# Kernel tuning notes

Measured on AMD Instinct MI355X. Metric: run time of the kernel, lower is better.

The kernel has to match this reference:

```python
import jax, jax.numpy as jnp
import numpy as np

C = 64
CQ = C // 8


def setup_inputs() -> dict:
    key = jax.random.key(0)
    ks = jax.random.split(key, 8)
    x = jax.random.normal(ks[0], (8, C, 64, 64), dtype=jnp.float32)
    s = 1.0 / np.sqrt(C)
    Wq = jax.random.normal(ks[1], (CQ, C), dtype=jnp.float32) * s
    bq = jax.random.normal(ks[2], (CQ,), dtype=jnp.float32) * s
    Wk = jax.random.normal(ks[3], (CQ, C), dtype=jnp.float32) * s
    bk = jax.random.normal(ks[4], (CQ,), dtype=jnp.float32) * s
    Wv = jax.random.normal(ks[5], (C, C), dtype=jnp.float32) * s
    bv = jax.random.normal(ks[6], (C,), dtype=jnp.float32) * s
    gamma = jnp.array([0.5], dtype=jnp.float32)  # nonzero so value path contributes
    return {"x": x, "Wq": Wq, "bq": bq, "Wk": Wk, "bk": bk, "Wv": Wv, "bv": bv, "gamma": gamma}


def reference(x, Wq, bq, Wk, bk, Wv, bv, gamma):
    B, Cc, H, W = x.shape
    xf = x.reshape(B, Cc, H * W)  # [B, C, N]
    # 1x1 conv == channel-mixing linear
    f = jnp.einsum('oc,bcn->bon', Wq, xf) + bq[None, :, None]  # [B, C/8, N]
    g = jnp.einsum('oc,bcn->bon', Wk, xf) + bk[None, :, None]  # [B, C/8, N]
    h = jnp.einsum('oc,bcn->bon', Wv, xf) + bv[None, :, None]  # [B, C, N]
    # scores[b,i,j] = f[b,:,i] . g[b,:,j]; softmax over dim=1 (query dim i)
    scores = jnp.einsum('bdi,bdj->bij', f, g)  # [B, N, N]
    beta = jax.nn.softmax(scores, axis=1)
    o = gamma[0] * jnp.einsum('bcn,bnm->bcm', h, beta) + xf
    return o.reshape(B, Cc, H, W)
```

## Files before the change

### kernel.cpp

```cpp
#include <hip/hip_runtime.h>
#include <hip/hip_fp16.h>


typedef _Float16 half8_t __attribute__((ext_vector_type(8)));
typedef _Float16 half4_t __attribute__((ext_vector_type(4)));
typedef _Float16 half2_t __attribute__((ext_vector_type(2)));
typedef __fp16  fp16x2  __attribute__((ext_vector_type(2)));
typedef float float4_t __attribute__((ext_vector_type(4)));
typedef unsigned int uintx4 __attribute__((ext_vector_type(4)));

#define NTOK 4096
#define PRH 72
#define LOG2E 1.44269504088896340736f

#if __has_builtin(__builtin_amdgcn_exp2f)
__device__ __forceinline__ float fexp2(float x) { return __builtin_amdgcn_exp2f(x); }
#else
__device__ __forceinline__ float fexp2(float x) { return exp2f(x); }
#endif

__device__ __forceinline__ half2_t pkcvt(float a, float b) {
    fp16x2 v = __builtin_amdgcn_cvt_pkrtz(a, b);
    return __builtin_bit_cast(half2_t, v);
}

__device__ __forceinline__ float4_t mfma16(half4_t a, half4_t b, float4_t c) {
    return __builtin_amdgcn_mfma_f32_16x16x16f16(a, b, c, 0, 0, 0);
}
__device__ __forceinline__ float4_t mfma32(half8_t a, half8_t b, float4_t c) {
    return __builtin_amdgcn_mfma_f32_16x16x32_f16(a, b, c, 0, 0, 0);
}

#define GLDS(G, L) __builtin_amdgcn_global_load_lds(                            \
    (const __attribute__((address_space(1))) unsigned int*)(G),                 \
    (__attribute__((address_space(3))) unsigned int*)(L), 16, 0, 0)

#define WAITVM4_BAR() do {                                                      \
    __builtin_amdgcn_sched_barrier(0);                                          \
    asm volatile("s_waitcnt vmcnt(4)" ::: "memory");                            \
    __builtin_amdgcn_sched_barrier(0);                                          \
    __builtin_amdgcn_s_barrier();                                               \
} while (0)

__global__ __launch_bounds__(320) void proj_kernel(
    const float* __restrict__ x,
    const float* __restrict__ Wq, const float* __restrict__ bq,
    const float* __restrict__ Wk, const float* __restrict__ bk,
    const float* __restrict__ Wv, const float* __restrict__ bv,
    __half* __restrict__ fTR, __half* __restrict__ gT16, __half* __restrict__ hM)
{
    __shared__ __align__(16) _Float16 xh[32 * PRH];
    const int t      = threadIdx.x;
    const int blk    = blockIdx.x;
    const int b      = blockIdx.y;
    const int n0     = blk * 32;
    const int kt64   = blk >> 1;
    const int t4base = (blk & 1) * 2;

    if (t < 256) {
#pragma unroll
        for (int i = 0; i < 2; i++) {
            const int idx = t + i * 256;
            const int c = idx >> 3, f4 = idx & 7;
            float4 v = *(const float4*)(x + (((size_t)(b * 64 + c)) << 12) + n0 + f4 * 4);
            const int cs = c ^ ((f4 & 3) << 4);
            xh[(f4 * 4 + 0) * PRH + cs] = (_Float16)v.x;
            xh[(f4 * 4 + 1) * PRH + cs] = (_Float16)v.y;
            xh[(f4 * 4 + 2) * PRH + cs] = (_Float16)v.z;
            xh[(f4 * 4 + 3) * PRH + cs] = (_Float16)v.w;
        }
    }

    const int w    = t >> 6;
    const int lane = t & 63;
    const int q    = lane >> 4;
    const int ml   = lane & 15;

    const float* wrow;
    if (w == 0) wrow = (ml < 8) ? (Wq + ml * 64) : (Wk + (ml - 8) * 64);
    else        wrow = Wv + ((w - 1) * 16 + ml) * 64;
    half4_t afr[4];
#pragma unroll
    for (int ks = 0; ks < 4; ks++) {
        float4 wv4 = *(const float4*)(wrow + ks * 16 + q * 4);
        afr[ks] = (half4_t){(_Float16)wv4.x, (_Float16)wv4.y,
                            (_Float16)wv4.z, (_Float16)wv4.w};
    }
    float4 bias4;
    if (w == 0) bias4 = (q < 2) ? *(const float4*)(bq + q * 4)
                                : *(const float4*)(bk + (q - 2) * 4);
    else        bias4 = *(const float4*)(bv + (w - 1) * 16 + q * 4);

    __syncthreads();

#pragma unroll
    for (int cg = 0; cg < 2; cg++) {
        const int tok  = cg * 16 + ml;
        const int swz  = (tok >> 2) & 3;
        float4_t acc = (float4_t){0.f, 0.f, 0.f, 0.f};
#pragma unroll
        for (int ks = 0; ks < 4; ks++) {
            half4_t bfr = *(const half4_t*)(&xh[tok * PRH + ((ks ^ swz) * 16 + q * 4)]);
            acc = __builtin_amdgcn_mfma_f32_16x16x16f16(afr[ks], bfr, acc, 0, 0, 0);
        }
        acc[0] += bias4.x; acc[1] += bias4.y; acc[2] += bias4.z; acc[3] += bias4.w;
        const int gtok = n0 + tok;
        const int t4   = t4base + cg;

        if (w == 0) {
            __half* rec = fTR + ((size_t)b << 16) + (size_t)(kt64 * 16 + ml) * 64;
            if (q < 2) {
                half4_t fv = {(_Float16)(acc[0] * LOG2E), (_Float16)(acc[1] * LOG2E),
                              (_Float16)(acc[2] * LOG2E), (_Float16)(acc[3] * LOG2E)};
                *(half4_t*)(rec + q * 16 + t4 * 4) = fv;
            } else {
                half4_t cv = (half4_t){};
                if (q == 2) cv[0] = (_Float16)1.0f;
                *(half4_t*)(rec + q * 16 + t4 * 4) = cv;
            }
            float gn2p = acc[0] * acc[0] + acc[1] * acc[1] +
                         acc[2] * acc[2] + acc[3] * acc[3];
            float gn2 = gn2p + __shfl_xor(gn2p, 16, 64);
            if (q >= 2) {
                half4_t gv = {(_Float16)acc[0], (_Float16)acc[1],
                              (_Float16)acc[2], (_Float16)acc[3]};
                __half* gp = gT16 + (size_t)((b << 12) + gtok) * 16;
                *(half4_t*)(gp + (q - 2) * 4) = gv;
                if (q == 2) {
                    const float M = (LOG2E * 4.6f) * __builtin_sqrtf(gn2) + 1.0f;
                    *(half4_t*)(gp + 8) = (half4_t){(_Float16)(-M), 0, 0, 0};
                } else {
                    *(half4_t*)(gp + 12) = (half4_t){};
                }
            }
        } else {
            const int ch  = (w - 1) * 16 + q * 4;
            const int pos = ((t4 >> 1) << 5) + ((ml >> 2) << 3) + ((t4 & 1) << 2) + (ml & 3);
            const size_t rowbase = ((size_t)(b * 64 + ch) << 12) + (size_t)kt64 * 64 + pos;
#pragma unroll
            for (int r = 0; r < 4; r++)
                hM[rowbase + ((size_t)r << 12)] = __float2half(acc[r]);
        }
    }
}

#define PAIR(SEA, SOA, SEB, SOB, HB, GOFF)                                      \
    {                                                                           \
        const _Float16* hp = (HB) + (GOFF);                                     \
        half8_t ah0 = *(const half8_t*)(hp);                                    \
        half8_t ah1 = *(const half8_t*)(hp + 1024);                             \
        half8_t ah2 = *(const half8_t*)(hp + 2048);                             \
        half8_t ah3 = *(const half8_t*)(hp + 3072);                             \
        float eA0 = fexp2(SEA[0]), eA1 = fexp2(SEA[1]),                         \
              eA2 = fexp2(SEA[2]), eA3 = fexp2(SEA[3]);                         \
        float oA0 = fexp2(SOA[0]), oA1 = fexp2(SOA[1]),                         \
              oA2 = fexp2(SOA[2]), oA3 = fexp2(SOA[3]);                         \
        float eB0 = fexp2(SEB[0]), eB1 = fexp2(SEB[1]),                         \
              eB2 = fexp2(SEB[2]), eB3 = fexp2(SEB[3]);                         \
        float oB0 = fexp2(SOB[0]), oB1 = fexp2(SOB[1]),                         \
              oB2 = fexp2(SOB[2]), oB3 = fexp2(SOB[3]);                         \
        uintx4 puA = {__builtin_bit_cast(unsigned int, pkcvt(eA0, eA1)),        \
                      __builtin_bit_cast(unsigned int, pkcvt(eA2, eA3)),        \
                      __builtin_bit_cast(unsigned int, pkcvt(oA0, oA1)),        \
                      __builtin_bit_cast(unsigned int, pkcvt(oA2, oA3))};       \
        uintx4 puB = {__builtin_bit_cast(unsigned int, pkcvt(eB0, eB1)),        \
                      __builtin_bit_cast(unsigned int, pkcvt(eB2, eB3)),        \
                      __builtin_bit_cast(unsigned int, pkcvt(oB0, oB1)),        \
                      __builtin_bit_cast(unsigned int, pkcvt(oB2, oB3))};       \
        half8_t pA8 = __builtin_bit_cast(half8_t, puA);                         \
        half8_t pB8 = __builtin_bit_cast(half8_t, puB);                         \
        __builtin_amdgcn_s_setprio(1);                                          \
        accLA = mfma32(ones8, pA8, accLA);                                      \
        accLB = mfma32(ones8, pB8, accLB);                                      \
        accA[0] = mfma32(ah0, pA8, accA[0]); accB[0] = mfma32(ah0, pB8, accB[0]); \
        accA[1] = mfma32(ah1, pA8, accA[1]); accB[1] = mfma32(ah1, pB8, accB[1]); \
        accA[2] = mfma32(ah2, pA8, accA[2]); accB[2] = mfma32(ah2, pB8, accB[2]); \
        accA[3] = mfma32(ah3, pA8, accA[3]); accB[3] = mfma32(ah3, pB8, accB[3]); \
        __builtin_amdgcn_s_setprio(0);                                          \
    }

template<int NT>
__global__ __launch_bounds__(256) void attn_kernel(
    const __half* __restrict__ fTR, const __half* __restrict__ gT16,
    const __half* __restrict__ hM,
    __half* __restrict__ Pacc, float* __restrict__ Lsum)
{
    __shared__ __align__(16) _Float16 hl[2][8192];
    const int tid   = threadIdx.x;
    const int w     = tid >> 6;
    const int lane  = tid & 63;
    const int q     = lane >> 4;
    const int ml    = lane & 15;
    const int m7    = ml & 7;
    const int b     = blockIdx.y;
    const int split = blockIdx.z;
    const int colA  = blockIdx.x * 128 + w * 16 + ml;
    const int colB  = colA + 64;

    half4_t gfA = *(const half4_t*)(gT16 + ((size_t)((b << 12) + colA)) * 16 + q * 4);
    half4_t gfB = *(const half4_t*)(gT16 + ((size_t)((b << 12) + colB)) * 16 + q * 4);

    float4_t accA[4], accB[4];
#pragma unroll
    for (int cg = 0; cg < 4; cg++) {
        accA[cg] = (float4_t){0.f, 0.f, 0.f, 0.f};
        accB[cg] = (float4_t){0.f, 0.f, 0.f, 0.f};
    }
    float4_t accLA = (float4_t){0.f, 0.f, 0.f, 0.f};
    float4_t accLB = (float4_t){0.f, 0.f, 0.f, 0.f};
    const half8_t ones8 = {(_Float16)1.0f, (_Float16)1.0f, (_Float16)1.0f,
                           (_Float16)1.0f, (_Float16)1.0f, (_Float16)1.0f,
                           (_Float16)1.0f, (_Float16)1.0f};
    const float4_t z4 = (float4_t){0.f, 0.f, 0.f, 0.f};

    const int k64 = split * NT * 2;

    const int ch0  = tid >> 3;
    const int gsw  = (tid & 7) ^ (ch0 & 7);
    const __half* hs0 = hM + ((size_t)(b * 64 + ch0) << 12) + (size_t)k64 * 64 + gsw * 8;
    const __half* hs1 = hs0 + ((size_t)32 << 12);
    const __half* fptr = fTR + ((size_t)b << 16) + (size_t)(k64 * 16 + ml) * 64 + q * 16;

    const int gxa = ((q ^ m7) << 3);
    const int gxb = (((4 + q) ^ m7) << 3);

    GLDS(hs0,      &hl[0][tid * 8]);
    GLDS(hs1,      &hl[0][2048 + tid * 8]);
    GLDS(hs0 + 64, &hl[0][4096 + tid * 8]);
    GLDS(hs1 + 64, &hl[0][6144 + tid * 8]);
    half8_t f01 = *(const half8_t*)fptr;
    half8_t f23 = *(const half8_t*)(fptr + 8);
    half8_t f45 = *(const half8_t*)(fptr + 1024);
    half8_t f67 = *(const half8_t*)(fptr + 1032);
    __syncthreads();

    const __half* hn0 = hs0 + 128;
    const __half* hn1 = hs1 + 128;

#pragma unroll 1
    for (int kt = 0; kt < NT; kt++) {
        if (kt + 1 < NT) {
            _Float16* nb = &hl[(kt + 1) & 1][0];
            GLDS(hn0,      nb + tid * 8);
            GLDS(hn1,      nb + 2048 + tid * 8);
            GLDS(hn0 + 64, nb + 4096 + tid * 8);
            GLDS(hn1 + 64, nb + 6144 + tid * 8);
            hn0 += 128;
            hn1 += 128;
        }

        const _Float16* hbA = &hl[kt & 1][ml << 6];
        const _Float16* hbB = hbA + 4096;

        {
            half4_t afn0 = __builtin_shufflevector(f01, f01, 0, 1, 2, 3);
            half4_t afn1 = __builtin_shufflevector(f01, f01, 4, 5, 6, 7);
            __builtin_amdgcn_s_setprio(1);
            float4_t stA0 = mfma16(afn0, gfA, z4);
            float4_t stB0 = mfma16(afn0, gfB, z4);
            float4_t stA1 = mfma16(afn1, gfA, z4);
            float4_t stB1 = mfma16(afn1, gfB, z4);
            __builtin_amdgcn_s_setprio(0);
            PAIR(stA0, stA1, stB0, stB1, hbA, gxa)

            half4_t afn2 = __builtin_shufflevector(f23, f23, 0, 1, 2, 3);
            half4_t afn3 = __builtin_shufflevector(f23, f23, 4, 5, 6, 7);
            __builtin_amdgcn_s_setprio(1);
            float4_t stA2 = mfma16(afn2, gfA, z4);
            float4_t stB2 = mfma16(afn2, gfB, z4);
            float4_t stA3 = mfma16(afn3, gfA, z4);
            float4_t stB3 = mfma16(afn3, gfB, z4);
            __builtin_amdgcn_s_setprio(0);
            if (kt + 1 < NT) {
                f01 = *(const half8_t*)(fptr + 2048);
                f23 = *(const half8_t*)(fptr + 2056);
            }
            PAIR(stA2, stA3, stB2, stB3, hbA, gxb)
        }

        {
            half4_t afn0 = __builtin_shufflevector(f45, f45, 0, 1, 2, 3);
            half4_t afn1 = __builtin_shufflevector(f45, f45, 4, 5, 6, 7);
            __builtin_amdgcn_s_setprio(1);
            float4_t stA0 = mfma16(afn0, gfA, z4);
            float4_t stB0 = mfma16(afn0, gfB, z4);
            float4_t stA1 = mfma16(afn1, gfA, z4);
            float4_t stB1 = mfma16(afn1, gfB, z4);
            __builtin_amdgcn_s_setprio(0);
            PAIR(stA0, stA1, stB0, stB1, hbB, gxa)

            half4_t afn2 = __builtin_shufflevector(f67, f67, 0, 1, 2, 3);
            half4_t afn3 = __builtin_shufflevector(f67, f67, 4, 5, 6, 7);
            __builtin_amdgcn_s_setprio(1);
            float4_t stA2 = mfma16(afn2, gfA, z4);
            float4_t stB2 = mfma16(afn2, gfB, z4);
            float4_t stA3 = mfma16(afn3, gfA, z4);
            float4_t stB3 = mfma16(afn3, gfB, z4);
            __builtin_amdgcn_s_setprio(0);
            if (kt + 1 < NT) {
                f45 = *(const half8_t*)(fptr + 3072);
                f67 = *(const half8_t*)(fptr + 3080);
                fptr += 2048;
            }
            PAIR(stA2, stA3, stB2, stB3, hbB, gxb)
        }

        if (kt + 1 < NT) {
            WAITVM4_BAR();
        }
    }

    __half* pa = Pacc + (((size_t)(split * 8 + b) * 64) << 12);
#pragma unroll
    for (int cg = 0; cg < 4; cg++)
#pragma unroll
        for (int r = 0; r < 4; r++) {
            int ch = cg * 16 + q * 4 + r;
            pa[((size_t)ch << 12) + colA] = __float2half(accA[cg][r]);
            pa[((size_t)ch << 12) + colB] = __float2half(accB[cg][r]);
        }
    if (q == 0) {
        Lsum[((size_t)(split * 8 + b) << 12) + colA] = accLA[0];
        Lsum[((size_t)(split * 8 + b) << 12) + colB] = accLB[0];
    }
}

template<int S>
__global__ __launch_bounds__(256) void merge_kernel(
    const __half* __restrict__ Pacc, const float* __restrict__ Lsum,
    const float* __restrict__ x, const float* __restrict__ gammap,
    float* __restrict__ out)
{
    __shared__ float invL[64];
    const int tid  = threadIdx.x;
    const int c4   = tid & 15;
    const int chh  = tid >> 4;
    const int b    = blockIdx.y;
    const int col0 = blockIdx.x * 64;
    const int ch   = blockIdx.z * 16 + chh;

    if (tid < 64) {
        float L = 0.f;
#pragma unroll
        for (int s = 0; s < S; s++)
            L += Lsum[((size_t)(s * 8 + b) << 12) + col0 + tid];
        invL[tid] = gammap[0] / L;
    }
    __syncthreads();

    const int cc = c4 * 4;
    const size_t base = (((size_t)b * 64 + ch) << 12) + col0 + cc;
    float4 xv = *(const float4*)(x + base);
    float o0 = 0.f, o1 = 0.f, o2 = 0.f, o3 = 0.f;
#pragma unroll
    for (int s = 0; s < S; s++) {
        half4_t pv = *(const half4_t*)(Pacc +
            (((size_t)(s * 8 + b) * 64 + ch) << 12) + col0 + cc);
        o0 += (float)pv[0];
        o1 += (float)pv[1];
        o2 += (float)pv[2];
        o3 += (float)pv[3];
    }
    float4 ov;
    ov.x = o0 * invL[cc]     + xv.x;
    ov.y = o1 * invL[cc + 1] + xv.y;
    ov.z = o2 * invL[cc + 2] + xv.z;
    ov.w = o3 * invL[cc + 3] + xv.w;
    *(float4*)(out + base) = ov;
}

extern "C" void kernel_launch(void* const* d_in, const int* in_sizes, int n_in,
                              void* d_out, int out_size, void* d_ws, size_t ws_size,
                              hipStream_t stream) {
    const float* x     = (const float*)d_in[0];
    const float* Wq    = (const float*)d_in[1];
    const float* bq    = (const float*)d_in[2];
    const float* Wk    = (const float*)d_in[3];
    const float* bk    = (const float*)d_in[4];
    const float* Wv    = (const float*)d_in[5];
    const float* bv    = (const float*)d_in[6];
    const float* gamma = (const float*)d_in[7];
    float* out = (float*)d_out;

    const size_t fr_bytes  = (size_t)8 * 65536 * 2;
    const size_t g_bytes   = (size_t)8 * NTOK * 16 * 2;
    const size_t hM_bytes  = (size_t)8 * 64 * NTOK * 2;
    const size_t pa_split  = (size_t)8 * 64 * NTOK * 2;
    const size_t l_split   = (size_t)8 * NTOK * sizeof(float);
    const size_t base_need = fr_bytes + g_bytes + hM_bytes;

    int S = 1;
    if (ws_size >= base_need + 4 * (pa_split + l_split)) S = 4;
    else if (ws_size >= base_need + 2 * (pa_split + l_split)) S = 2;

    char* p = (char*)d_ws;
    __half* fTR  = (__half*)p;  p += fr_bytes;
    __half* gT16 = (__half*)p;  p += g_bytes;
    __half* hM   = (__half*)p;  p += hM_bytes;
    __half* Pacc = (__half*)p;  p += (size_t)S * pa_split;
    float*  Lsum = (float*)p;

    proj_kernel<<<dim3(128, 8), 320, 0, stream>>>(x, Wq, bq, Wk, bk, Wv, bv,
                                                  fTR, gT16, hM);
    if (S == 4) {
        attn_kernel<8><<<dim3(32, 8, 4), 256, 0, stream>>>(fTR, gT16, hM, Pacc, Lsum);
        merge_kernel<4><<<dim3(64, 8, 4), 256, 0, stream>>>(Pacc, Lsum, x, gamma, out);
    } else if (S == 2) {
        attn_kernel<16><<<dim3(32, 8, 2), 256, 0, stream>>>(fTR, gT16, hM, Pacc, Lsum);
        merge_kernel<2><<<dim3(64, 8, 4), 256, 0, stream>>>(Pacc, Lsum, x, gamma, out);
    } else {
        attn_kernel<32><<<dim3(32, 8, 1), 256, 0, stream>>>(fTR, gT16, hM, Pacc, Lsum);
        merge_kernel<1><<<dim3(64, 8, 4), 256, 0, stream>>>(Pacc, Lsum, x, gamma, out);
    }
}
```

Before: 116.5 us.

## Coalesce h stores via LDS transpose and software-pipeline attention loop loads

```diff
diff --git a/kernel.cpp b/kernel.cpp
--- a/kernel.cpp
+++ b/kernel.cpp
@@ -93,6 +93,7 @@
 
     __syncthreads();
 
+    float4_t acc2[2];
 #pragma unroll
     for (int cg = 0; cg < 2; cg++) {
         const int tok  = cg * 16 + ml;
@@ -104,6 +105,7 @@
             acc = __builtin_amdgcn_mfma_f32_16x16x16f16(afr[ks], bfr, acc, 0, 0, 0);
         }
         acc[0] += bias4.x; acc[1] += bias4.y; acc[2] += bias4.z; acc[3] += bias4.w;
+        acc2[cg] = acc;
         const int gtok = n0 + tok;
         const int t4   = t4base + cg;
 
@@ -133,32 +135,61 @@
                     *(half4_t*)(gp + 12) = (half4_t){};
                 }
             }
-        } else {
-            const int ch  = (w - 1) * 16 + q * 4;
-            const int pos = ((t4 >> 1) << 5) + ((ml >> 2) << 3) + ((t4 & 1) << 2) + (ml & 3);
-            const size_t rowbase = ((size_t)(b * 64 + ch) << 12) + (size_t)kt64 * 64 + pos;
+        }
+    }
+
+    __syncthreads();
+    if (w > 0) {
+        const int ch = (w - 1) * 16 + q * 4;
+#pragma unroll
+        for (int cg = 0; cg < 2; cg++) {
+            const int loc = ((ml >> 2) << 3) + (cg << 2) + (ml & 3);
 #pragma unroll
             for (int r = 0; r < 4; r++)
-                hM[rowbase + ((size_t)r << 12)] = __float2half(acc[r]);
-        }
-    }
-}
-
-#define PAIR(SEA, SOA, SEB, SOB, HB, GOFF)                                      \
+                xh[(ch + r) * 36 + loc] = (_Float16)acc2[cg][r];
+        }
+    }
+    __syncthreads();
+    if (t < 256) {
+        const int ch   = t >> 2;
+        const int part = t & 3;
+        half8_t v = *(const half8_t*)(&xh[ch * 36 + part * 8]);
+        __half* dst = hM + ((size_t)(b * 64 + ch) << 12) + (size_t)kt64 * 64
+                         + (blk & 1) * 32 + part * 8;
+        *(half8_t*)dst = v;
+    }
+}
+
+
+#define LDAH(V0, V1, V2, V3, HP)                                                \
+    half8_t V0 = *(const half8_t*)(HP);                                         \
+    half8_t V1 = *(const half8_t*)((HP) + 1024);                                \
+    half8_t V2 = *(const half8_t*)((HP) + 2048);                                \
+    half8_t V3 = *(const half8_t*)((HP) + 3072);
+
+#define QK(F, N)                                                                \
+    float4_t N##A0, N##B0, N##A1, N##B1;                                        \
     {                                                                           \
-        const _Float16* hp = (HB) + (GOFF);                                     \
-        half8_t ah0 = *(const half8_t*)(hp);                                    \
-        half8_t ah1 = *(const half8_t*)(hp + 1024);                             \
-        half8_t ah2 = *(const half8_t*)(hp + 2048);                             \
-        half8_t ah3 = *(const half8_t*)(hp + 3072);                             \
-        float eA0 = fexp2(SEA[0]), eA1 = fexp2(SEA[1]),                         \
-              eA2 = fexp2(SEA[2]), eA3 = fexp2(SEA[3]);                         \
-        float oA0 = fexp2(SOA[0]), oA1 = fexp2(SOA[1]),                         \
-              oA2 = fexp2(SOA[2]), oA3 = fexp2(SOA[3]);                         \
-        float eB0 = fexp2(SEB[0]), eB1 = fexp2(SEB[1]),                         \
-              eB2 = fexp2(SEB[2]), eB3 = fexp2(SEB[3]);                         \
-        float oB0 = fexp2(SOB[0]), oB1 = fexp2(SOB[1]),                         \
-              oB2 = fexp2(SOB[2]), oB3 = fexp2(SOB[3]);                         \
+        half4_t a0 = __builtin_shufflevector(F, F, 0, 1, 2, 3);                 \
+        half4_t a1 = __builtin_shufflevector(F, F, 4, 5, 6, 7);                 \
+        __builtin_amdgcn_s_setprio(1);                                          \
+        N##A0 = mfma16(a0, gfA, z4);                                            \
+        N##B0 = mfma16(a0, gfB, z4);                                            \
+        N##A1 = mfma16(a1, gfA, z4);                                            \
+        N##B1 = mfma16(a1, gfB, z4);                                            \
+        __builtin_amdgcn_s_setprio(0);                                          \
+    }
+
+#define PAIRC(N, H0, H1, H2, H3)                                                \
+    {                                                                           \
+        float eA0 = fexp2(N##A0[0]), eA1 = fexp2(N##A0[1]),                     \
+              eA2 = fexp2(N##A0[2]), eA3 = fexp2(N##A0[3]);                     \
+        float oA0 = fexp2(N##A1[0]), oA1 = fexp2(N##A1[1]),                     \
+              oA2 = fexp2(N##A1[2]), oA3 = fexp2(N##A1[3]);                     \
+        float eB0 = fexp2(N##B0[0]), eB1 = fexp2(N##B0[1]),                     \
+              eB2 = fexp2(N##B0[2]), eB3 = fexp2(N##B0[3]);                     \
+        float oB0 = fexp2(N##B1[0]), oB1 = fexp2(N##B1[1]),                     \
+              oB2 = fexp2(N##B1[2]), oB3 = fexp2(N##B1[3]);                     \
         uintx4 puA = {__builtin_bit_cast(unsigned int, pkcvt(eA0, eA1)),        \
                       __builtin_bit_cast(unsigned int, pkcvt(eA2, eA3)),        \
                       __builtin_bit_cast(unsigned int, pkcvt(oA0, oA1)),        \
@@ -172,10 +203,10 @@
         __builtin_amdgcn_s_setprio(1);                                          \
         accLA = mfma32(ones8, pA8, accLA);                                      \
         accLB = mfma32(ones8, pB8, accLB);                                      \
-        accA[0] = mfma32(ah0, pA8, accA[0]); accB[0] = mfma32(ah0, pB8, accB[0]); \
-        accA[1] = mfma32(ah1, pA8, accA[1]); accB[1] = mfma32(ah1, pB8, accB[1]); \
-        accA[2] = mfma32(ah2, pA8, accA[2]); accB[2] = mfma32(ah2, pB8, accB[2]); \
-        accA[3] = mfma32(ah3, pA8, accA[3]); accB[3] = mfma32(ah3, pB8, accB[3]); \
+        accA[0] = mfma32(H0, pA8, accA[0]); accB[0] = mfma32(H0, pB8, accB[0]); \
+        accA[1] = mfma32(H1, pA8, accA[1]); accB[1] = mfma32(H1, pB8, accB[1]); \
+        accA[2] = mfma32(H2, pA8, accA[2]); accB[2] = mfma32(H2, pB8, accB[2]); \
+        accA[3] = mfma32(H3, pA8, accA[3]); accB[3] = mfma32(H3, pB8, accB[3]); \
         __builtin_amdgcn_s_setprio(0);                                          \
     }
 
@@ -239,6 +270,12 @@
 
 #pragma unroll 1
     for (int kt = 0; kt < NT; kt++) {
+        const _Float16* hbA = &hl[kt & 1][ml << 6];
+        const _Float16* hbB = hbA + 4096;
+
+        LDAH(a00, a01, a02, a03, hbA + gxa)
+        QK(f01, s)
+
         if (kt + 1 < NT) {
             _Float16* nb = &hl[(kt + 1) & 1][0];
             GLDS(hn0,      nb + tid * 8);
@@ -249,61 +286,30 @@
             hn1 += 128;
         }
 
-        const _Float16* hbA = &hl[kt & 1][ml << 6];
-        const _Float16* hbB = hbA + 4096;
-
-        {
-            half4_t afn0 = __builtin_shufflevector(f01, f01, 0, 1, 2, 3);
-            half4_t afn1 = __builtin_shufflevector(f01, f01, 4, 5, 6, 7);
-            __builtin_amdgcn_s_setprio(1);
-            float4_t stA0 = mfma16(afn0, gfA, z4);
-            float4_t stB0 = mfma16(afn0, gfB, z4);
-            float4_t stA1 = mfma16(afn1, gfA, z4);
-            float4_t stB1 = mfma16(afn1, gfB, z4);
-            __builtin_amdgcn_s_setprio(0);
-            PAIR(stA0, stA1, stB0, stB1, hbA, gxa)
-
-            half4_t afn2 = __builtin_shufflevector(f23, f23, 0, 1, 2, 3);
-            half4_t afn3 = __builtin_shufflevector(f23, f23, 4, 5, 6, 7);
-            __builtin_amdgcn_s_setprio(1);
-            float4_t stA2 = mfma16(afn2, gfA, z4);
-            float4_t stB2 = mfma16(afn2, gfB, z4);
-            float4_t stA3 = mfma16(afn3, gfA, z4);
-            float4_t stB3 = mfma16(afn3, gfB, z4);
-            __builtin_amdgcn_s_setprio(0);
-            if (kt + 1 < NT) {
-                f01 = *(const half8_t*)(fptr + 2048);
-                f23 = *(const half8_t*)(fptr + 2056);
-            }
-            PAIR(stA2, stA3, stB2, stB3, hbA, gxb)
-        }
-
-        {
-            half4_t afn0 = __builtin_shufflevector(f45, f45, 0, 1, 2, 3);
-            half4_t afn1 = __builtin_shufflevector(f45, f45, 4, 5, 6, 7);
-            __builtin_amdgcn_s_setprio(1);
-            float4_t stA0 = mfma16(afn0, gfA, z4);
-            float4_t stB0 = mfma16(afn0, gfB, z4);
-            float4_t stA1 = mfma16(afn1, gfA, z4);
-            float4_t stB1 = mfma16(afn1, gfB, z4);
-            __builtin_amdgcn_s_setprio(0);
-            PAIR(stA0, stA1, stB0, stB1, hbB, gxa)
-
-            half4_t afn2 = __builtin_shufflevector(f67, f67, 0, 1, 2, 3);
-            half4_t afn3 = __builtin_shufflevector(f67, f67, 4, 5, 6, 7);
-            __builtin_amdgcn_s_setprio(1);
-            float4_t stA2 = mfma16(afn2, gfA, z4);
-            float4_t stB2 = mfma16(afn2, gfB, z4);
-            float4_t stA3 = mfma16(afn3, gfA, z4);
-            float4_t stB3 = mfma16(afn3, gfB, z4);
-            __builtin_amdgcn_s_setprio(0);
-            if (kt + 1 < NT) {
-                f45 = *(const half8_t*)(fptr + 3072);
-                f67 = *(const half8_t*)(fptr + 3080);
-                fptr += 2048;
-            }
-            PAIR(stA2, stA3, stB2, stB3, hbB, gxb)
-        }
+        LDAH(a10, a11, a12, a13, hbA + gxb)
+        QK(f23, t)
+
+        PAIRC(s, a00, a01, a02, a03)
+
+        LDAH(a20, a21, a22, a23, hbB + gxa)
+
+        PAIRC(t, a10, a11, a12, a13)
+
+        QK(f45, u)
+        LDAH(a30, a31, a32, a33, hbB + gxb)
+
+        PAIRC(u, a20, a21, a22, a23)
+
+        QK(f67, v)
+        if (kt + 1 < NT) {
+            f01 = *(const half8_t*)(fptr + 2048);
+            f23 = *(const half8_t*)(fptr + 2056);
+            f45 = *(const half8_t*)(fptr + 3072);
+            f67 = *(const half8_t*)(fptr + 3080);
+            fptr += 2048;
+        }
+
+        PAIRC(v, a30, a31, a32, a33)
 
         if (kt + 1 < NT) {
             WAITVM4_BAR();
```

New measurement: 114.5 us. Within noise of the previous version (-1.7%).
